# Kernel tuning notes

Hardware: AMD Instinct MI355X
Metric: run time of the kernel (lower is better)

Reference implementation:

```python
import jax, jax.numpy as jnp
import numpy as np

VOXEL = 0.1  # voxel size used in NSLoss.voxelize


def _chamfer(x, y):
    """Squared-distance chamfer terms. x: [B,N,3], y: [B,M,3].
    Returns (dist1 [B,N]: min over y for each x point, dist2 [B,M])."""
    xx = jnp.sum(x * x, axis=-1)              # [B,N]
    yy = jnp.sum(y * y, axis=-1)              # [B,M]
    zz = jnp.einsum('bnd,bmd->bnm', x, y)     # [B,N,M]
    P = xx[:, :, None] + yy[None if False else slice(None), None, :][0] if False else xx[:, :, None] + yy[:, None, :] - 2.0 * zz
    return P.min(axis=2), P.min(axis=1)


def _voxelize(coord):
    # masked_fill(nan -> inf), per-batch min over points, quantize, truncate to int
    c = jnp.where(jnp.isnan(coord), jnp.inf, coord)
    gmin = c.min(axis=1, keepdims=True)       # [B,1,3]
    grid = ((coord - gmin) / VOXEL).astype(jnp.int32)  # trunc like torch .int()
    return jax.lax.stop_gradient(grid)        # torch .int() detaches grad


def setup_inputs() -> dict:
    key = jax.random.key(0)
    k1, k2 = jax.random.split(key)
    preds = jax.random.normal(k1, (2, 8192, 3), dtype=jnp.float32)
    gts = jax.random.normal(k2, (2, 8192, 3), dtype=jnp.float32)
    return {"preds": preds, "gts": gts}


def reference(preds, gts):
    # chamfer on raw coordinates
    d1, d2 = _chamfer(preds, gts)
    loss2 = d1.mean() + d2.mean()
    # chamfer on voxelized coordinates
    pv = _voxelize(preds).astype(jnp.float32)
    gv = _voxelize(gts).astype(jnp.float32)
    d1v, d2v = _chamfer(pv, gv)
    loss1 = d1v.mean() + d2v.mean()
    return loss1 + loss2
```

## Files before the change

kernel.cpp:

```cpp
#include <hip/hip_runtime.h>
#include <math.h>

#define B 2
#define N 8192
#define PTS_STRIDE (N*3)
#define VOXEL 0.1f

#define BLK  256
#define PBLK 1024
#define XPB 64
#define XTILES (N/XPB)
#define NBLOCKS (XTILES*4)
#define CH 128

#define WS_GMIN 0
#define WS_ACC 16
#define WS_TICKET 17
#define OFF_PACK 32
#define PERG 147456
#define OFF_AF(g)  (OFF_PACK + (g)*PERG)
#define OFF_BR(g)  (OFF_AF(g) + 65536)
#define OFF_BV(g)  (OFF_BR(g) + 32768)
#define OFF_XXR(g) (OFF_BV(g) + 32768)
#define OFF_XXV(g) (OFF_XXR(g) + 8192)

typedef __attribute__((ext_vector_type(8))) short short8;
typedef __attribute__((ext_vector_type(16))) float f16v;

union S8 { short8 v; unsigned short u[8]; };

__device__ __forceinline__ unsigned short f2bf(float f) {
    unsigned u = __float_as_uint(f);
    return (unsigned short)((u + 0x7FFFu + ((u >> 16) & 1u)) >> 16);
}
__device__ __forceinline__ float bf2f(unsigned short h) {
    return __uint_as_float(((unsigned)h) << 16);
}
__device__ __forceinline__ float voxq(float v, float g) {
    return (float)(int)((v - g) / VOXEL);
}

__global__ void __launch_bounds__(PBLK)
gmin_kernel(const float* __restrict__ preds,
            const float* __restrict__ gts,
            float* __restrict__ ws) {
    const int g   = blockIdx.x;
    const int arr = g >> 1;
    const int b   = g & 1;
    const float* base = (arr ? gts : preds) + b * PTS_STRIDE;

    float m0 = INFINITY, m1 = INFINITY, m2 = INFINITY;
    for (int i = threadIdx.x; i < N; i += PBLK) {
        float v0 = base[i*3+0], v1 = base[i*3+1], v2 = base[i*3+2];
        v0 = (v0 != v0) ? INFINITY : v0;
        v1 = (v1 != v1) ? INFINITY : v1;
        v2 = (v2 != v2) ? INFINITY : v2;
        m0 = fminf(m0, v0); m1 = fminf(m1, v1); m2 = fminf(m2, v2);
    }
    for (int off = 32; off; off >>= 1) {
        m0 = fminf(m0, __shfl_down(m0, off));
        m1 = fminf(m1, __shfl_down(m1, off));
        m2 = fminf(m2, __shfl_down(m2, off));
    }
    __shared__ float sm[16][3];
    const int wave = threadIdx.x >> 6, lane = threadIdx.x & 63;
    if (lane == 0) { sm[wave][0] = m0; sm[wave][1] = m1; sm[wave][2] = m2; }
    __syncthreads();
    if (threadIdx.x == 0) {
        float a0 = sm[0][0], a1 = sm[0][1], a2 = sm[0][2];
        for (int w = 1; w < 16; ++w) {
            a0 = fminf(a0, sm[w][0]);
            a1 = fminf(a1, sm[w][1]);
            a2 = fminf(a2, sm[w][2]);
        }
        ws[WS_GMIN + g*3+0] = a0; ws[WS_GMIN + g*3+1] = a1; ws[WS_GMIN + g*3+2] = a2;
        if (g == 0) { ws[WS_ACC] = 0.0f; ((unsigned*)ws)[WS_TICKET] = 0u; }
    }
}

__global__ void __launch_bounds__(BLK)
pack_kernel(const float* __restrict__ preds,
            const float* __restrict__ gts,
            float* __restrict__ ws) {
    const int i   = blockIdx.x * BLK + threadIdx.x;
    const int g   = i >> 13;
    const int idx = i & (N-1);
    const int arr = g >> 1;
    const int b   = g & 1;
    const float* base = (arr ? gts : preds) + b * PTS_STRIDE;

    const float g0 = ws[WS_GMIN + g*3+0];
    const float g1 = ws[WS_GMIN + g*3+1];
    const float g2 = ws[WS_GMIN + g*3+2];

    const float p0 = base[idx*3+0], p1 = base[idx*3+1], p2 = base[idx*3+2];
    const float w0 = voxq(p0, g0), w1 = voxq(p1, g1), w2 = voxq(p2, g2);
    const float rr = fmaf(p0,p0, fmaf(p1,p1, p2*p2));
    const float vv = fmaf(w0,w0, fmaf(w1,w1, w2*w2));

    const unsigned short yyh = f2bf(rr);
    const unsigned short yyl = f2bf(rr - bf2f(yyh));
    const unsigned short vvh = f2bf(vv);
    const unsigned short vvl = f2bf(vv - bf2f(vvh));
    const unsigned short ONE = 0x3F80;

    short8* AF = (short8*)(ws + OFF_AF(g));
    short8* BR = (short8*)(ws + OFF_BR(g));
    short8* BV = (short8*)(ws + OFF_BV(g));

    S8 f;
    f.u[0]=f2bf(p0); f.u[1]=f2bf(p1); f.u[2]=f2bf(p2);
    f.u[3]=yyh; f.u[4]=yyl; f.u[5]=f2bf(w0); f.u[6]=f2bf(w1); f.u[7]=f2bf(w2);
    AF[idx*2] = f.v;
    f.u[0]=vvh; f.u[1]=vvl; f.u[2]=0; f.u[3]=0; f.u[4]=0; f.u[5]=0; f.u[6]=0; f.u[7]=0;
    AF[idx*2+1] = f.v;
    f.u[0]=f2bf(-2.0f*p0); f.u[1]=f2bf(-2.0f*p1); f.u[2]=f2bf(-2.0f*p2);
    f.u[3]=ONE; f.u[4]=ONE; f.u[5]=0; f.u[6]=0; f.u[7]=0;
    BR[idx] = f.v;
    f.u[0]=0; f.u[1]=0; f.u[2]=0; f.u[3]=0; f.u[4]=0;
    f.u[5]=f2bf(-2.0f*w0); f.u[6]=f2bf(-2.0f*w1); f.u[7]=f2bf(-2.0f*w2);
    BV[idx] = f.v;
    ws[OFF_XXR(g) + idx] = rr;
    ws[OFF_XXV(g) + idx] = vv;
}

__global__ void __launch_bounds__(BLK, 2)
chamfer_kernel(float* __restrict__ ws, float* __restrict__ out) {
    const int tid  = threadIdx.x;
    const int wave = tid >> 6, lane = tid & 63;
    const int half = lane >> 5, c32 = lane & 31;
    const int slot = blockIdx.y;
    const int dir  = slot & 1;
    const int b    = slot >> 1;
    const int gX = dir*2 + b;
    const int gY = (1-dir)*2 + b;

    const short8* AF = (const short8*)(ws + OFF_AF(gY));
    const short8* BR = (const short8*)(ws + OFF_BR(gX));
    const short8* BV = (const short8*)(ws + OFF_BV(gX));

    __shared__ short8 lds[4][CH*2];
    __shared__ float smin[4][4][32];
    __shared__ float ssum[2];

    const int xbase = blockIdx.x * XPB;
    short8 bf[4];
    S8 hc;
    hc.u[0] = (c32 < 16) ? (unsigned short)0 : (unsigned short)0x3F80;
    hc.u[1] = hc.u[0];
    hc.u[2]=0; hc.u[3]=0; hc.u[4]=0; hc.u[5]=0; hc.u[6]=0; hc.u[7]=0;
#pragma unroll
    for (int f = 0; f < 4; ++f) {
        const int xi = xbase + f*16 + (c32 & 15);
        if (half == 0) {
            bf[f] = (c32 < 16) ? BR[xi] : BV[xi];
        } else {
            bf[f] = hc.v;
        }
    }

    float mn0 = INFINITY, mn1 = INFINITY, mn2 = INFINITY, mn3 = INFINITY;
    const f16v Z = (f16v)(0.0f);
    const int ybase = wave * 2048;

    for (int c = 0; c < 2048/CH; ++c) {
        const int fbase = (ybase + c*CH) * 2;
#pragma unroll
        for (int j = 0; j < 4; ++j)
            lds[wave][lane + j*64] = AF[fbase + lane + j*64];

#pragma unroll
        for (int t = 0; t < CH/32; ++t) {
            const short8 a = lds[wave][(t*32 + c32)*2 + half];
            const f16v d0 = __builtin_amdgcn_mfma_f32_32x32x16_bf16(a, bf[0], Z, 0, 0, 0);
            const f16v d1 = __builtin_amdgcn_mfma_f32_32x32x16_bf16(a, bf[1], Z, 0, 0, 0);
            const f16v d2 = __builtin_amdgcn_mfma_f32_32x32x16_bf16(a, bf[2], Z, 0, 0, 0);
            const f16v d3 = __builtin_amdgcn_mfma_f32_32x32x16_bf16(a, bf[3], Z, 0, 0, 0);
#pragma unroll
            for (int r = 0; r < 16; r += 4) {
                mn0 = fminf(mn0, fminf(fminf(d0[r], d0[r+1]), fminf(d0[r+2], d0[r+3])));
                mn1 = fminf(mn1, fminf(fminf(d1[r], d1[r+1]), fminf(d1[r+2], d1[r+3])));
                mn2 = fminf(mn2, fminf(fminf(d2[r], d2[r+1]), fminf(d2[r+2], d2[r+3])));
                mn3 = fminf(mn3, fminf(fminf(d3[r], d3[r+1]), fminf(d3[r+2], d3[r+3])));
            }
        }
    }

    mn0 = fminf(mn0, __shfl_xor(mn0, 32));
    mn1 = fminf(mn1, __shfl_xor(mn1, 32));
    mn2 = fminf(mn2, __shfl_xor(mn2, 32));
    mn3 = fminf(mn3, __shfl_xor(mn3, 32));
    if (half == 0) {
        smin[wave][0][c32] = mn0;
        smin[wave][1][c32] = mn1;
        smin[wave][2][c32] = mn2;
        smin[wave][3][c32] = mn3;
    }
    __syncthreads();

    if (tid < 128) {
        const int f   = tid >> 5;
        const int col = tid & 31;
        float v = fminf(fminf(smin[0][f][col], smin[1][f][col]),
                        fminf(smin[2][f][col], smin[3][f][col]));
        const int xi = xbase + f*16 + (col & 15);
        v += (col < 16) ? ws[OFF_XXR(gX) + xi] : ws[OFF_XXV(gX) + xi];
        for (int off = 32; off; off >>= 1)
            v += __shfl_down(v, off);
        if ((tid & 63) == 0) ssum[tid >> 6] = v;
    }
    __syncthreads();
    if (tid == 0) {
        const float bs = ssum[0] + ssum[1];
        atomicAdd(ws + WS_ACC, bs);
        __threadfence();
        const unsigned t = atomicAdd(&((unsigned*)ws)[WS_TICKET], 1u);
        if (t == NBLOCKS - 1) {
            __threadfence();
            const float total = atomicAdd(ws + WS_ACC, 0.0f);
            out[0] = total * (1.0f / 16384.0f);
        }
    }
}

extern "C" void kernel_launch(void* const* d_in, const int* in_sizes, int n_in,
                              void* d_out, int out_size, void* d_ws, size_t ws_size,
                              hipStream_t stream) {
    const float* preds = (const float*)d_in[0];
    const float* gts   = (const float*)d_in[1];
    float* ws  = (float*)d_ws;
    float* out = (float*)d_out;

    gmin_kernel<<<dim3(4), dim3(PBLK), 0, stream>>>(preds, gts, ws);
    pack_kernel<<<dim3(128), dim3(BLK), 0, stream>>>(preds, gts, ws);
    chamfer_kernel<<<dim3(XTILES, 4), dim3(BLK), 0, stream>>>(ws, out);
}
```

Measured before the change: 97.29 us.

## Split packed A into lo/hi planes, drop LDS staging, use 8 waves per block

The packed A operand is split into separate low and high planes so each half-wave can load its MFMA fragment directly from global memory. This removes the per-wave LDS staging copy. Blocks grow to 512 threads (8 waves), so each wave scans 1024 y points instead of 2048, and the final reduction now combines 8 per-wave partial minima. The aim is to cut LDS round trips and raise parallelism per block, at the cost of relying on cache-served global loads inside the MFMA loop and higher register pressure from launch bounds of 4.

```diff
diff --git a/kernel.cpp b/kernel.cpp
--- a/kernel.cpp
+++ b/kernel.cpp
@@ -6,23 +6,23 @@
 #define PTS_STRIDE (N*3)
 #define VOXEL 0.1f
 
-#define BLK  256
+#define BLK  512
 #define PBLK 1024
 #define XPB 64
 #define XTILES (N/XPB)
 #define NBLOCKS (XTILES*4)
-#define CH 128
 
 #define WS_GMIN 0
 #define WS_ACC 16
 #define WS_TICKET 17
 #define OFF_PACK 32
 #define PERG 147456
-#define OFF_AF(g)  (OFF_PACK + (g)*PERG)
-#define OFF_BR(g)  (OFF_AF(g) + 65536)
-#define OFF_BV(g)  (OFF_BR(g) + 32768)
-#define OFF_XXR(g) (OFF_BV(g) + 32768)
-#define OFF_XXV(g) (OFF_XXR(g) + 8192)
+#define OFF_AFLO(g) (OFF_PACK + (g)*PERG)
+#define OFF_AFHI(g) (OFF_AFLO(g) + 32768)
+#define OFF_BR(g)   (OFF_AFLO(g) + 65536)
+#define OFF_BV(g)   (OFF_AFLO(g) + 98304)
+#define OFF_XXR(g)  (OFF_AFLO(g) + 131072)
+#define OFF_XXV(g)  (OFF_AFLO(g) + 139264)
 
 typedef __attribute__((ext_vector_type(8))) short short8;
 typedef __attribute__((ext_vector_type(16))) float f16v;
@@ -78,11 +78,11 @@
     }
 }
 
-__global__ void __launch_bounds__(BLK)
+__global__ void __launch_bounds__(256)
 pack_kernel(const float* __restrict__ preds,
             const float* __restrict__ gts,
             float* __restrict__ ws) {
-    const int i   = blockIdx.x * BLK + threadIdx.x;
+    const int i   = blockIdx.x * 256 + threadIdx.x;
     const int g   = i >> 13;
     const int idx = i & (N-1);
     const int arr = g >> 1;
@@ -104,16 +104,17 @@
     const unsigned short vvl = f2bf(vv - bf2f(vvh));
     const unsigned short ONE = 0x3F80;
 
-    short8* AF = (short8*)(ws + OFF_AF(g));
-    short8* BR = (short8*)(ws + OFF_BR(g));
-    short8* BV = (short8*)(ws + OFF_BV(g));
+    short8* AFLO = (short8*)(ws + OFF_AFLO(g));
+    short8* AFHI = (short8*)(ws + OFF_AFHI(g));
+    short8* BR   = (short8*)(ws + OFF_BR(g));
+    short8* BV   = (short8*)(ws + OFF_BV(g));
 
     S8 f;
     f.u[0]=f2bf(p0); f.u[1]=f2bf(p1); f.u[2]=f2bf(p2);
     f.u[3]=yyh; f.u[4]=yyl; f.u[5]=f2bf(w0); f.u[6]=f2bf(w1); f.u[7]=f2bf(w2);
-    AF[idx*2] = f.v;
+    AFLO[idx] = f.v;
     f.u[0]=vvh; f.u[1]=vvl; f.u[2]=0; f.u[3]=0; f.u[4]=0; f.u[5]=0; f.u[6]=0; f.u[7]=0;
-    AF[idx*2+1] = f.v;
+    AFHI[idx] = f.v;
     f.u[0]=f2bf(-2.0f*p0); f.u[1]=f2bf(-2.0f*p1); f.u[2]=f2bf(-2.0f*p2);
     f.u[3]=ONE; f.u[4]=ONE; f.u[5]=0; f.u[6]=0; f.u[7]=0;
     BR[idx] = f.v;
@@ -124,7 +125,7 @@
     ws[OFF_XXV(g) + idx] = vv;
 }
 
-__global__ void __launch_bounds__(BLK, 2)
+__global__ void __launch_bounds__(BLK, 4)
 chamfer_kernel(float* __restrict__ ws, float* __restrict__ out) {
     const int tid  = threadIdx.x;
     const int wave = tid >> 6, lane = tid & 63;
@@ -135,12 +136,13 @@
     const int gX = dir*2 + b;
     const int gY = (1-dir)*2 + b;
 
-    const short8* AF = (const short8*)(ws + OFF_AF(gY));
+    const short8* ALO = (const short8*)(ws + OFF_AFLO(gY));
+    const short8* AHI = (const short8*)(ws + OFF_AFHI(gY));
+    const short8* Abase = half ? AHI : ALO;
     const short8* BR = (const short8*)(ws + OFF_BR(gX));
     const short8* BV = (const short8*)(ws + OFF_BV(gX));
 
-    __shared__ short8 lds[4][CH*2];
-    __shared__ float smin[4][4][32];
+    __shared__ float smin[8][4][32];
     __shared__ float ssum[2];
 
     const int xbase = blockIdx.x * XPB;
@@ -152,37 +154,26 @@
 #pragma unroll
     for (int f = 0; f < 4; ++f) {
         const int xi = xbase + f*16 + (c32 & 15);
-        if (half == 0) {
-            bf[f] = (c32 < 16) ? BR[xi] : BV[xi];
-        } else {
-            bf[f] = hc.v;
-        }
+        bf[f] = (half == 0) ? ((c32 < 16) ? BR[xi] : BV[xi]) : hc.v;
     }
 
     float mn0 = INFINITY, mn1 = INFINITY, mn2 = INFINITY, mn3 = INFINITY;
     const f16v Z = (f16v)(0.0f);
-    const int ybase = wave * 2048;
-
-    for (int c = 0; c < 2048/CH; ++c) {
-        const int fbase = (ybase + c*CH) * 2;
+    const int abase0 = wave * 1024 + c32;
+
+#pragma unroll 2
+    for (int t = 0; t < 32; ++t) {
+        const short8 a = Abase[abase0 + t*32];
+        const f16v d0 = __builtin_amdgcn_mfma_f32_32x32x16_bf16(a, bf[0], Z, 0, 0, 0);
+        const f16v d1 = __builtin_amdgcn_mfma_f32_32x32x16_bf16(a, bf[1], Z, 0, 0, 0);
+        const f16v d2 = __builtin_amdgcn_mfma_f32_32x32x16_bf16(a, bf[2], Z, 0, 0, 0);
+        const f16v d3 = __builtin_amdgcn_mfma_f32_32x32x16_bf16(a, bf[3], Z, 0, 0, 0);
 #pragma unroll
-        for (int j = 0; j < 4; ++j)
-            lds[wave][lane + j*64] = AF[fbase + lane + j*64];
-
-#pragma unroll
-        for (int t = 0; t < CH/32; ++t) {
-            const short8 a = lds[wave][(t*32 + c32)*2 + half];
-            const f16v d0 = __builtin_amdgcn_mfma_f32_32x32x16_bf16(a, bf[0], Z, 0, 0, 0);
-            const f16v d1 = __builtin_amdgcn_mfma_f32_32x32x16_bf16(a, bf[1], Z, 0, 0, 0);
-            const f16v d2 = __builtin_amdgcn_mfma_f32_32x32x16_bf16(a, bf[2], Z, 0, 0, 0);
-            const f16v d3 = __builtin_amdgcn_mfma_f32_32x32x16_bf16(a, bf[3], Z, 0, 0, 0);
-#pragma unroll
-            for (int r = 0; r < 16; r += 4) {
-                mn0 = fminf(mn0, fminf(fminf(d0[r], d0[r+1]), fminf(d0[r+2], d0[r+3])));
-                mn1 = fminf(mn1, fminf(fminf(d1[r], d1[r+1]), fminf(d1[r+2], d1[r+3])));
-                mn2 = fminf(mn2, fminf(fminf(d2[r], d2[r+1]), fminf(d2[r+2], d2[r+3])));
-                mn3 = fminf(mn3, fminf(fminf(d3[r], d3[r+1]), fminf(d3[r+2], d3[r+3])));
-            }
+        for (int r = 0; r < 16; r += 4) {
+            mn0 = fminf(mn0, fminf(fminf(d0[r], d0[r+1]), fminf(d0[r+2], d0[r+3])));
+            mn1 = fminf(mn1, fminf(fminf(d1[r], d1[r+1]), fminf(d1[r+2], d1[r+3])));
+            mn2 = fminf(mn2, fminf(fminf(d2[r], d2[r+1]), fminf(d2[r+2], d2[r+3])));
+            mn3 = fminf(mn3, fminf(fminf(d3[r], d3[r+1]), fminf(d3[r+2], d3[r+3])));
         }
     }
 
@@ -201,8 +192,9 @@
     if (tid < 128) {
         const int f   = tid >> 5;
         const int col = tid & 31;
-        float v = fminf(fminf(smin[0][f][col], smin[1][f][col]),
-                        fminf(smin[2][f][col], smin[3][f][col]));
+        float v = smin[0][f][col];
+#pragma unroll
+        for (int w = 1; w < 8; ++w) v = fminf(v, smin[w][f][col]);
         const int xi = xbase + f*16 + (col & 15);
         v += (col < 16) ? ws[OFF_XXR(gX) + xi] : ws[OFF_XXV(gX) + xi];
         for (int off = 32; off; off >>= 1)
@@ -232,6 +224,6 @@
     float* out = (float*)d_out;
 
     gmin_kernel<<<dim3(4), dim3(PBLK), 0, stream>>>(preds, gts, ws);
-    pack_kernel<<<dim3(128), dim3(BLK), 0, stream>>>(preds, gts, ws);
+    pack_kernel<<<dim3(128), dim3(256), 0, stream>>>(preds, gts, ws);
     chamfer_kernel<<<dim3(XTILES, 4), dim3(BLK), 0, stream>>>(ws, out);
 }
```

New measurement: 96.04 us. No clear change (-1.3%).
